# Performance work log

Hardware: AMD Instinct MI355X
Metric: run time of the kernel (lower is better)

The kernel has to match this reference:

```python
import jax, jax.numpy as jnp
import numpy as np
import math

B, T, C = 2, 2048, 1024
H = 16
D = C // H

def setup_inputs() -> dict:
    key = jax.random.key(0)
    k1, k2, k3, k4, k5 = jax.random.split(key, 5)
    scale = 0.02
    return {
        "x": jax.random.normal(k1, (B, T, C), dtype=jnp.float32),
        "w_attn": jax.random.normal(k2, (3 * C, C), dtype=jnp.float32) * scale,
        "b_attn": jax.random.normal(k3, (3 * C,), dtype=jnp.float32) * scale,
        "w_proj": jax.random.normal(k4, (C, C), dtype=jnp.float32) * scale,
        "b_proj": jax.random.normal(k5, (C,), dtype=jnp.float32) * scale,
    }

def reference(x, w_attn, b_attn, w_proj, b_proj):
    b, t, c = x.shape
    # c_attn: torch Linear -> x @ W.T + b, output [b, t, 3c]
    qkv = jnp.einsum('btc,fc->btf', x, w_attn) + b_attn
    # einops 'b t (a h d) -> a b h t d' with a=3, h=H
    qkv = qkv.reshape(b, t, 3, H, D).transpose(2, 0, 3, 1, 4)
    q, k, v = qkv[0], qkv[1], qkv[2]  # each [b, h, t, d]
    att = jnp.einsum('bhtd,bhsd->bhts', q, k) * (1.0 / math.sqrt(D))
    # causal mask: positions s > t are masked
    mask = jnp.tril(jnp.ones((t, t), dtype=bool))
    att = jnp.where(mask[None, None, :, :], att, jnp.float32(-jnp.inf))
    att = jax.nn.softmax(att, axis=-1)
    y = jnp.einsum('bhts,bhsd->bhtd', att, v)  # [b, h, t, d]
    y = y.transpose(0, 2, 1, 3).reshape(b, t, c)
    return jnp.einsum('btc,fc->btf', y, w_proj) + b_proj
```

## Files before the change

### kernel.cpp

```cpp
#include <hip/hip_runtime.h>
#include <hip/hip_bf16.h>
#include <stdint.h>

typedef unsigned short u16;
typedef __attribute__((ext_vector_type(8))) __bf16 bvec8;
typedef __attribute__((ext_vector_type(4))) float f32x4;
typedef __attribute__((ext_vector_type(16))) float f32x16;

__device__ __forceinline__ u16 f32_to_bf16(float f) {
    uint32_t u = __float_as_uint(f);
    u += 0x7fffu + ((u >> 16) & 1u);
    return (u16)(u >> 16);
}
__device__ __forceinline__ uint32_t pack_bf16x2(float lo, float hi) {
    union { __hip_bfloat162 h; uint32_t u; } c;
    c.h = __float22bfloat162_rn(make_float2(lo, hi));
    return c.u;
}

__device__ __forceinline__ void gl2lds16(const u16* g, u16* l) {
    void* gnc = const_cast<void*>((const void*)g);
    __builtin_amdgcn_global_load_lds(
        (__attribute__((address_space(1))) uint32_t*)gnc,
        (__attribute__((address_space(3))) uint32_t*)((void*)l),
        16, 0, 0);
}

__global__ __launch_bounds__(256) void cvt3(
    const float* __restrict__ a, int na4, const float* __restrict__ b, int nb4,
    const float* __restrict__ c, int nc4,
    u16* __restrict__ oa, u16* __restrict__ ob, u16* __restrict__ oc)
{
    int i = blockIdx.x * 256 + threadIdx.x;
    const float* src; u16* dst; int off;
    if (i < na4)             { src = a; dst = oa; off = i; }
    else if (i < na4 + nb4)  { src = b; dst = ob; off = i - na4; }
    else if (i < na4 + nb4 + nc4) { src = c; dst = oc; off = i - na4 - nb4; }
    else return;
    float4 v = ((const float4*)src)[off];
    ushort4 o;
    o.x = f32_to_bf16(v.x); o.y = f32_to_bf16(v.y);
    o.z = f32_to_bf16(v.z); o.w = f32_to_bf16(v.w);
    ((ushort4*)dst)[off] = o;
}

template <int BNt, bool OUT_BF16>
__global__ __launch_bounds__(256) void gemm_bt_bias(
    const u16* __restrict__ A, const u16* __restrict__ B,
    const float* __restrict__ bias, void* __restrict__ Cv,
    int M, int N, int K)
{
    constexpr int NT = BNt / 32;
    __shared__ __attribute__((aligned(16))) u16 As[128 * 32];
    __shared__ __attribute__((aligned(16))) u16 Bs[BNt * 32];

    const int tid = threadIdx.x, wave = tid >> 6, lane = tid & 63;
    const int col = lane & 15, quad = lane >> 4;
    const int m0 = blockIdx.y * 128, n0 = blockIdx.x * BNt;
    const int wm = (wave >> 1) * 64, wn = (wave & 1) * (BNt / 2);
    const int srow = lane >> 2, schunk = lane & 3;
    const u16* Ag = A + (size_t)(m0 + wave * 32) * K;

    f32x4 acc[4][NT];
#pragma unroll
    for (int i = 0; i < 4; i++)
#pragma unroll
        for (int j = 0; j < NT; j++) acc[i][j] = f32x4{0.f, 0.f, 0.f, 0.f};

    for (int k0 = 0; k0 < K; k0 += 32) {
        __syncthreads();
        gl2lds16(Ag + (size_t)(srow)      * K + k0 + schunk * 8, &As[(wave * 2 + 0) * 512]);
        gl2lds16(Ag + (size_t)(16 + srow) * K + k0 + schunk * 8, &As[(wave * 2 + 1) * 512]);
        if constexpr (BNt == 128) {
            const u16* Bg = B + (size_t)(n0 + wave * 32) * K;
            gl2lds16(Bg + (size_t)(srow)      * K + k0 + schunk * 8, &Bs[(wave * 2 + 0) * 512]);
            gl2lds16(Bg + (size_t)(16 + srow) * K + k0 + schunk * 8, &Bs[(wave * 2 + 1) * 512]);
        } else {
            const u16* Bg = B + (size_t)(n0 + wave * 16) * K;
            gl2lds16(Bg + (size_t)(srow)      * K + k0 + schunk * 8, &Bs[wave * 512]);
        }
        __syncthreads();

        bvec8 af[4], bfv[NT];
#pragma unroll
        for (int mt = 0; mt < 4; mt++)  af[mt]  = *(const bvec8*)&As[(wm + mt * 16 + col) * 32 + quad * 8];
#pragma unroll
        for (int nt = 0; nt < NT; nt++) bfv[nt] = *(const bvec8*)&Bs[(wn + nt * 16 + col) * 32 + quad * 8];
#pragma unroll
        for (int mt = 0; mt < 4; mt++)
#pragma unroll
            for (int nt = 0; nt < NT; nt++)
                acc[mt][nt] = __builtin_amdgcn_mfma_f32_16x16x32_bf16(af[mt], bfv[nt], acc[mt][nt], 0, 0, 0);
    }

#pragma unroll
    for (int mt = 0; mt < 4; mt++) {
#pragma unroll
        for (int r = 0; r < 4; r++) {
            const int m = m0 + wm + mt * 16 + quad * 4 + r;
#pragma unroll
            for (int nt = 0; nt < NT; nt++) {
                const int n = n0 + wn + nt * 16 + col;
                float v = acc[mt][nt][r] + bias[n];
                if (OUT_BF16) ((u16*)Cv)[(size_t)m * N + n] = f32_to_bf16(v);
                else          ((float*)Cv)[(size_t)m * N + n] = v;
            }
        }
    }
}

__global__ __launch_bounds__(256) void transpose_v(const u16* __restrict__ qkv,
                                                   u16* __restrict__ vT)
{
    __shared__ u16 Ts[64 * 74];
    const int tid = threadIdx.x;
    const int t0 = blockIdx.x * 64, h = blockIdx.y, b = blockIdx.z;
    const u16* src = qkv + (size_t)b * 2048 * 3072 + 2048 + h * 64;
#pragma unroll
    for (int k2 = 0; k2 < 2; k2++) {
        int c = k2 * 256 + tid, tl = c >> 3, ch = c & 7;
        *(uint4*)&Ts[tl * 74 + ch * 8] = *(const uint4*)(src + (size_t)(t0 + tl) * 3072 + ch * 8);
    }
    __syncthreads();
    u16* dst = vT + (size_t)((b * 16 + h) * 64) * 2048;
#pragma unroll
    for (int k2 = 0; k2 < 2; k2++) {
        int c = k2 * 256 + tid, d = c >> 3, tch = c & 7;
        u16 tmp[8];
#pragma unroll
        for (int j2 = 0; j2 < 8; j2++) {
            int p  = tch * 8 + j2;
            int sl = (p & 32) | ((p & 1) << 4) | ((p >> 1) & 15);
            tmp[j2] = Ts[sl * 74 + d];
        }
        *(uint4*)&dst[(size_t)d * 2048 + t0 + tch * 8] = *(const uint4*)tmp;
    }
}

__global__ __launch_bounds__(256) void attn_kernel(const u16* __restrict__ qkv,
                                                   const u16* __restrict__ vT,
                                                   u16* __restrict__ Y)
{
    __shared__ __attribute__((aligned(16))) u16 Qs[64 * 64];
    __shared__ __attribute__((aligned(16))) u16 Ks[2][64 * 64];
    __shared__ __attribute__((aligned(16))) u16 Vs[2][64 * 64];
    __shared__ __attribute__((aligned(16))) float Obuf[2][64][36];
    __shared__ __attribute__((aligned(16))) float Lbuf[2][2][32];

    const int tid = threadIdx.x, wave = tid >> 6, lane = tid & 63;
    const int l31 = lane & 31, hi = lane >> 5;
    const int wq = wave >> 1, ws = wave & 1;

    const int g = blockIdx.x;
    const int b = g >> 4, h = g & 15;
    const int s_idx = blockIdx.y;

    const u16* qb = qkv + (size_t)b * 2048 * 3072;
    const u16* vb = vT + (size_t)g * 64 * 2048;

    const int c0 = wave * 64 + lane, c1 = 256 + c0;
    const int r0 = c0 >> 3, p0c = c0 & 7, r1 = c1 >> 3, p1c = c1 & 7;
    const int sw0 = (p0c ^ (r0 & 7)) * 8, sw1 = (p1c ^ (r1 & 7)) * 8;

    const int q_lane = wq * 32 + l31;
    const int s_lane = ws * 32 + l31;

#pragma unroll
    for (int phase = 0; phase < 2; ++phase) {
        const int qt = phase ? (31 - s_idx) : s_idx;
        const int q0 = qt * 64;

        __syncthreads();
        gl2lds16(qb + (size_t)(q0 + r0) * 3072 + h * 64 + sw0, &Qs[wave * 512]);
        gl2lds16(qb + (size_t)(q0 + r1) * 3072 + h * 64 + sw1, &Qs[2048 + wave * 512]);
        gl2lds16(qb + (size_t)(r0) * 3072 + 1024 + h * 64 + sw0, &Ks[0][wave * 512]);
        gl2lds16(qb + (size_t)(r1) * 3072 + 1024 + h * 64 + sw1, &Ks[0][2048 + wave * 512]);
        gl2lds16(vb + (size_t)r0 * 2048 + sw0, &Vs[0][wave * 512]);
        gl2lds16(vb + (size_t)r1 * 2048 + sw1, &Vs[0][2048 + wave * 512]);
        asm volatile("s_waitcnt vmcnt(4)" ::: "memory");
        asm volatile("s_barrier" ::: "memory");

        bvec8 qf[4];
#pragma unroll
        for (int c = 0; c < 4; c++)
            qf[c] = *(const bvec8*)&Qs[q_lane * 64 + (((c * 2 + hi) ^ (q_lane & 7)) * 8)];

        float l_acc = 0.f;
        f32x16 o0, o1;
#pragma unroll
        for (int i = 0; i < 16; i++) { o0[i] = 0.f; o1[i] = 0.f; }

        for (int kt = 0; kt <= qt; ++kt) {
            const int cur = kt & 1;
            if (kt < qt) {
                const int s0n = (kt + 1) * 64, nb2 = cur ^ 1;
                gl2lds16(qb + (size_t)(s0n + r0) * 3072 + 1024 + h * 64 + sw0, &Ks[nb2][wave * 512]);
                gl2lds16(qb + (size_t)(s0n + r1) * 3072 + 1024 + h * 64 + sw1, &Ks[nb2][2048 + wave * 512]);
                gl2lds16(vb + (size_t)r0 * 2048 + s0n + sw0, &Vs[nb2][wave * 512]);
                gl2lds16(vb + (size_t)r1 * 2048 + s0n + sw1, &Vs[nb2][2048 + wave * 512]);
                asm volatile("s_waitcnt vmcnt(4)" ::: "memory");
            } else {
                asm volatile("s_waitcnt vmcnt(0)" ::: "memory");
            }
            asm volatile("s_barrier" ::: "memory");

            const bool diag = (kt == qt);
            if (!(diag && wq == 0 && ws == 1)) {
                f32x16 sv;
#pragma unroll
                for (int i = 0; i < 16; i++) sv[i] = 0.f;
#pragma unroll
                for (int c = 0; c < 4; c++) {
                    bvec8 kf = *(const bvec8*)&Ks[cur][s_lane * 64 + (((c * 2 + hi) ^ (s_lane & 7)) * 8)];
                    sv = __builtin_amdgcn_mfma_f32_32x32x16_bf16(kf, qf[c], sv, 0, 0, 0);
                }

                float pv[16];
                if (diag) {
                    const int s_base = kt * 64 + ws * 32 + 4 * hi;
                    const int q_act  = q0 + wq * 32 + l31;
#pragma unroll
                    for (int i = 0; i < 16; i++) {
                        float p = exp2f(sv[i] * 0.1803368801f);
                        int s_act = s_base + (i & 3) + 8 * (i >> 2);
                        if (s_act > q_act) p = 0.f;
                        pv[i] = p;
                    }
                } else {
#pragma unroll
                    for (int i = 0; i < 16; i++)
                        pv[i] = exp2f(sv[i] * 0.1803368801f);
                }
                {
                    float t0a = (pv[0] + pv[1]) + (pv[2] + pv[3]);
                    float t1a = (pv[4] + pv[5]) + (pv[6] + pv[7]);
                    float t2a = (pv[8] + pv[9]) + (pv[10] + pv[11]);
                    float t3a = (pv[12] + pv[13]) + (pv[14] + pv[15]);
                    l_acc += (t0a + t1a) + (t2a + t3a);
                }

                uint32_t w[8];
#pragma unroll
                for (int i = 0; i < 8; i++) w[i] = pack_bf16x2(pv[i], pv[i + 8]);
                union { uint32_t u[4]; bvec8 v; } pf0, pf1;
                pf0.u[0] = w[0]; pf0.u[1] = w[1]; pf0.u[2] = w[2]; pf0.u[3] = w[3];
                pf1.u[0] = w[4]; pf1.u[1] = w[5]; pf1.u[2] = w[6]; pf1.u[3] = w[7];

#pragma unroll
                for (int ch = 0; ch < 2; ch++) {
                    bvec8 pf = ch ? pf1.v : pf0.v;
                    const int lc = ws * 4 + ch * 2 + hi;
                    const int d0r = l31;
                    bvec8 vf0 = *(const bvec8*)&Vs[cur][d0r * 64 + ((lc ^ (d0r & 7)) * 8)];
                    o0 = __builtin_amdgcn_mfma_f32_32x32x16_bf16(pf, vf0, o0, 0, 0, 0);
                    const int d1r = 32 + l31;
                    bvec8 vf1 = *(const bvec8*)&Vs[cur][d1r * 64 + ((lc ^ (d1r & 7)) * 8)];
                    o1 = __builtin_amdgcn_mfma_f32_32x32x16_bf16(pf, vf1, o1, 0, 0, 0);
                }
            }
            asm volatile("s_barrier" ::: "memory");
        }

        l_acc += __shfl_xor(l_acc, 32);
        __syncthreads();
        if (lane < 32) Lbuf[ws][wq][lane] = l_acc;
        if (ws == 0) {
#pragma unroll
            for (int nt = 0; nt < 2; nt++) {
                const int d = nt * 32 + l31;
#pragma unroll
                for (int g4 = 0; g4 < 4; g4++) {
                    f32x4 v;
#pragma unroll
                    for (int j = 0; j < 4; j++) v[j] = nt ? o1[g4 * 4 + j] : o0[g4 * 4 + j];
                    *(f32x4*)&Obuf[wq][d][8 * g4 + 4 * hi] = v;
                }
            }
        }
        __syncthreads();
        if (ws == 1) {
            float inv[16];
#pragma unroll
            for (int g4 = 0; g4 < 4; g4++) {
                f32x4 la = *(const f32x4*)&Lbuf[0][wq][8 * g4 + 4 * hi];
                f32x4 lb = *(const f32x4*)&Lbuf[1][wq][8 * g4 + 4 * hi];
#pragma unroll
                for (int j = 0; j < 4; j++) inv[g4 * 4 + j] = 1.0f / (la[j] + lb[j]);
            }
#pragma unroll
            for (int nt = 0; nt < 2; nt++) {
                const int d = nt * 32 + l31;
#pragma unroll
                for (int g4 = 0; g4 < 4; g4++) {
                    f32x4 po = *(const f32x4*)&Obuf[wq][d][8 * g4 + 4 * hi];
#pragma unroll
                    for (int j = 0; j < 4; j++) {
                        const int i = g4 * 4 + j;
                        float val = ((nt ? o1[i] : o0[i]) + po[j]) * inv[i];
                        const int t = q0 + wq * 32 + 8 * g4 + 4 * hi + j;
                        Y[(size_t)(b * 2048 + t) * 1024 + h * 64 + d] = f32_to_bf16(val);
                    }
                }
            }
        }
    }
}

extern "C" void kernel_launch(void* const* d_in, const int* in_sizes, int n_in,
                              void* d_out, int out_size, void* d_ws, size_t ws_size,
                              hipStream_t stream) {
    const float* x      = (const float*)d_in[0];
    const float* w_attn = (const float*)d_in[1];
    const float* b_attn = (const float*)d_in[2];
    const float* w_proj = (const float*)d_in[3];
    const float* b_proj = (const float*)d_in[4];
    float* out = (float*)d_out;

    u16* xb  = (u16*)d_ws;
    u16* wab = xb  + (size_t)4096 * 1024;
    u16* wpb = wab + (size_t)3072 * 1024;
    u16* qkv = wpb + (size_t)1024 * 1024;
    u16* y   = qkv + (size_t)4096 * 3072;
    u16* vT  = xb;

    const int na4 = 4096 * 1024 / 4, nb4 = 3072 * 1024 / 4, nc4 = 1024 * 1024 / 4;
    cvt3<<<(na4 + nb4 + nc4 + 255) / 256, 256, 0, stream>>>(
        x, na4, w_attn, nb4, w_proj, nc4, xb, wab, wpb);

    dim3 g1(3072 / 128, 4096 / 128);
    gemm_bt_bias<128, true><<<g1, 256, 0, stream>>>(xb, wab, b_attn, qkv, 4096, 3072, 1024);

    dim3 gt(32, 16, 2);
    transpose_v<<<gt, 256, 0, stream>>>(qkv, vT);

    dim3 g2(32, 16, 1);
    attn_kernel<<<g2, 256, 0, stream>>>(qkv, vT, y);

    dim3 g3(1024 / 64, 4096 / 128);
    gemm_bt_bias<64, false><<<g3, 256, 0, stream>>>(y, wpb, b_proj, out, 4096, 1024, 1024);
}
```

Measured before the change: 194.3 us.

## Use 128-row query tiles with one wave per 32 queries in attention

The attention kernel now gives each block a 128-query tile, with each of the four waves owning 32 query rows across the full 64-key tile. This replaces the old 64-query tiles, where two waves split the keys and merged partial outputs through shared memory. Load balancing now pairs tile j with tile 23-j. Each K/V tile loaded into shared memory is reused by twice as many queries, and the cross-wave Obuf/Lbuf reduction and its syncthreads are gone. In exchange there are fewer blocks (a grid y of 16 is implied), which may lower occupancy, and each wave holds more registers.

Result: slower. 210.1 us (+8.2%).

```diff
diff --git a/kernel.cpp b/kernel.cpp
--- a/kernel.cpp
+++ b/kernel.cpp
@@ -141,167 +141,143 @@
                                                    const u16* __restrict__ vT,
                                                    u16* __restrict__ Y)
 {
-    __shared__ __attribute__((aligned(16))) u16 Qs[64 * 64];
+    __shared__ __attribute__((aligned(16))) u16 Qs[128 * 64];
     __shared__ __attribute__((aligned(16))) u16 Ks[2][64 * 64];
     __shared__ __attribute__((aligned(16))) u16 Vs[2][64 * 64];
-    __shared__ __attribute__((aligned(16))) float Obuf[2][64][36];
-    __shared__ __attribute__((aligned(16))) float Lbuf[2][2][32];
+    __shared__ __attribute__((aligned(16))) float Lbuf[4][32];
 
     const int tid = threadIdx.x, wave = tid >> 6, lane = tid & 63;
     const int l31 = lane & 31, hi = lane >> 5;
-    const int wq = wave >> 1, ws = wave & 1;
 
     const int g = blockIdx.x;
     const int b = g >> 4, h = g & 15;
-    const int s_idx = blockIdx.y;
+    const int j = blockIdx.y;
+    const int qt = (j < 8) ? j : (23 - j);
+    const int q0 = qt * 128;
+    const int nkt = 2 * qt + 2;
 
     const u16* qb = qkv + (size_t)b * 2048 * 3072;
     const u16* vb = vT + (size_t)g * 64 * 2048;
 
+#pragma unroll
+    for (int g4 = 0; g4 < 4; g4++) {
+        int c = g4 * 256 + wave * 64 + lane;
+        int r = c >> 3, ch = c & 7;
+        gl2lds16(qb + (size_t)(q0 + r) * 3072 + h * 64 + ((ch ^ (r & 7)) * 8),
+                 &Qs[g4 * 2048 + wave * 512]);
+    }
     const int c0 = wave * 64 + lane, c1 = 256 + c0;
-    const int r0 = c0 >> 3, p0c = c0 & 7, r1 = c1 >> 3, p1c = c1 & 7;
-    const int sw0 = (p0c ^ (r0 & 7)) * 8, sw1 = (p1c ^ (r1 & 7)) * 8;
-
-    const int q_lane = wq * 32 + l31;
-    const int s_lane = ws * 32 + l31;
-
-#pragma unroll
-    for (int phase = 0; phase < 2; ++phase) {
-        const int qt = phase ? (31 - s_idx) : s_idx;
-        const int q0 = qt * 64;
-
-        __syncthreads();
-        gl2lds16(qb + (size_t)(q0 + r0) * 3072 + h * 64 + sw0, &Qs[wave * 512]);
-        gl2lds16(qb + (size_t)(q0 + r1) * 3072 + h * 64 + sw1, &Qs[2048 + wave * 512]);
-        gl2lds16(qb + (size_t)(r0) * 3072 + 1024 + h * 64 + sw0, &Ks[0][wave * 512]);
-        gl2lds16(qb + (size_t)(r1) * 3072 + 1024 + h * 64 + sw1, &Ks[0][2048 + wave * 512]);
-        gl2lds16(vb + (size_t)r0 * 2048 + sw0, &Vs[0][wave * 512]);
-        gl2lds16(vb + (size_t)r1 * 2048 + sw1, &Vs[0][2048 + wave * 512]);
-        asm volatile("s_waitcnt vmcnt(4)" ::: "memory");
+    const int r0 = c0 >> 3, r1 = c1 >> 3;
+    const int sw0 = ((c0 & 7) ^ (r0 & 7)) * 8, sw1 = ((c1 & 7) ^ (r1 & 7)) * 8;
+
+    gl2lds16(qb + (size_t)(r0) * 3072 + 1024 + h * 64 + sw0, &Ks[0][wave * 512]);
+    gl2lds16(qb + (size_t)(r1) * 3072 + 1024 + h * 64 + sw1, &Ks[0][2048 + wave * 512]);
+    gl2lds16(vb + (size_t)r0 * 2048 + sw0, &Vs[0][wave * 512]);
+    gl2lds16(vb + (size_t)r1 * 2048 + sw1, &Vs[0][2048 + wave * 512]);
+    asm volatile("s_waitcnt vmcnt(4)" ::: "memory");
+    asm volatile("s_barrier" ::: "memory");
+
+    const int q_lane = wave * 32 + l31;
+    bvec8 qf[4];
+#pragma unroll
+    for (int c = 0; c < 4; c++)
+        qf[c] = *(const bvec8*)&Qs[q_lane * 64 + (((c * 2 + hi) ^ (q_lane & 7)) * 8)];
+
+    const int qmin  = q0 + wave * 32;
+    const int qmax  = qmin + 31;
+    const int q_act = qmin + l31;
+
+    float l_acc = 0.f;
+    f32x16 o0, o1;
+#pragma unroll
+    for (int i = 0; i < 16; i++) { o0[i] = 0.f; o1[i] = 0.f; }
+
+    for (int kt = 0; kt < nkt; ++kt) {
+        const int cur = kt & 1;
+        if (kt + 1 < nkt) {
+            const int s0n = (kt + 1) * 64, nb2 = cur ^ 1;
+            gl2lds16(qb + (size_t)(s0n + r0) * 3072 + 1024 + h * 64 + sw0, &Ks[nb2][wave * 512]);
+            gl2lds16(qb + (size_t)(s0n + r1) * 3072 + 1024 + h * 64 + sw1, &Ks[nb2][2048 + wave * 512]);
+            gl2lds16(vb + (size_t)r0 * 2048 + s0n + sw0, &Vs[nb2][wave * 512]);
+            gl2lds16(vb + (size_t)r1 * 2048 + s0n + sw1, &Vs[nb2][2048 + wave * 512]);
+            asm volatile("s_waitcnt vmcnt(4)" ::: "memory");
+        } else {
+            asm volatile("s_waitcnt vmcnt(0)" ::: "memory");
+        }
         asm volatile("s_barrier" ::: "memory");
 
-        bvec8 qf[4];
-#pragma unroll
-        for (int c = 0; c < 4; c++)
-            qf[c] = *(const bvec8*)&Qs[q_lane * 64 + (((c * 2 + hi) ^ (q_lane & 7)) * 8)];
-
-        float l_acc = 0.f;
-        f32x16 o0, o1;
-#pragma unroll
-        for (int i = 0; i < 16; i++) { o0[i] = 0.f; o1[i] = 0.f; }
-
-        for (int kt = 0; kt <= qt; ++kt) {
-            const int cur = kt & 1;
-            if (kt < qt) {
-                const int s0n = (kt + 1) * 64, nb2 = cur ^ 1;
-                gl2lds16(qb + (size_t)(s0n + r0) * 3072 + 1024 + h * 64 + sw0, &Ks[nb2][wave * 512]);
-                gl2lds16(qb + (size_t)(s0n + r1) * 3072 + 1024 + h * 64 + sw1, &Ks[nb2][2048 + wave * 512]);
-                gl2lds16(vb + (size_t)r0 * 2048 + s0n + sw0, &Vs[nb2][wave * 512]);
-                gl2lds16(vb + (size_t)r1 * 2048 + s0n + sw1, &Vs[nb2][2048 + wave * 512]);
-                asm volatile("s_waitcnt vmcnt(4)" ::: "memory");
-            } else {
-                asm volatile("s_waitcnt vmcnt(0)" ::: "memory");
-            }
-            asm volatile("s_barrier" ::: "memory");
-
-            const bool diag = (kt == qt);
-            if (!(diag && wq == 0 && ws == 1)) {
-                f32x16 sv;
-#pragma unroll
-                for (int i = 0; i < 16; i++) sv[i] = 0.f;
-#pragma unroll
-                for (int c = 0; c < 4; c++) {
-                    bvec8 kf = *(const bvec8*)&Ks[cur][s_lane * 64 + (((c * 2 + hi) ^ (s_lane & 7)) * 8)];
-                    sv = __builtin_amdgcn_mfma_f32_32x32x16_bf16(kf, qf[c], sv, 0, 0, 0);
+        const int s_t0 = kt * 64;
+        if (s_t0 <= qmax) {
+            f32x16 sv0, sv1;
+#pragma unroll
+            for (int i = 0; i < 16; i++) { sv0[i] = 0.f; sv1[i] = 0.f; }
+#pragma unroll
+            for (int c = 0; c < 4; c++) {
+                bvec8 kf = *(const bvec8*)&Ks[cur][l31 * 64 + (((c * 2 + hi) ^ (l31 & 7)) * 8)];
+                sv0 = __builtin_amdgcn_mfma_f32_32x32x16_bf16(kf, qf[c], sv0, 0, 0, 0);
+            }
+#pragma unroll
+            for (int c = 0; c < 4; c++) {
+                const int rr = 32 + l31;
+                bvec8 kf = *(const bvec8*)&Ks[cur][rr * 64 + (((c * 2 + hi) ^ (rr & 7)) * 8)];
+                sv1 = __builtin_amdgcn_mfma_f32_32x32x16_bf16(kf, qf[c], sv1, 0, 0, 0);
+            }
+
+            const bool msk = (s_t0 + 63 > qmin);
+            float pv0[16], pv1[16];
+#pragma unroll
+            for (int i = 0; i < 16; i++) {
+                float p0 = __expf(sv0[i] * 0.125f);
+                float p1 = __expf(sv1[i] * 0.125f);
+                if (msk) {
+                    const int srow = s_t0 + (i & 3) + 8 * (i >> 2) + 4 * hi;
+                    if (srow > q_act)      p0 = 0.f;
+                    if (srow + 32 > q_act) p1 = 0.f;
                 }
-
-                float pv[16];
-                if (diag) {
-                    const int s_base = kt * 64 + ws * 32 + 4 * hi;
-                    const int q_act  = q0 + wq * 32 + l31;
-#pragma unroll
-                    for (int i = 0; i < 16; i++) {
-                        float p = exp2f(sv[i] * 0.1803368801f);
-                        int s_act = s_base + (i & 3) + 8 * (i >> 2);
-                        if (s_act > q_act) p = 0.f;
-                        pv[i] = p;
-                    }
-                } else {
-#pragma unroll
-                    for (int i = 0; i < 16; i++)
-                        pv[i] = exp2f(sv[i] * 0.1803368801f);
-                }
-                {
-                    float t0a = (pv[0] + pv[1]) + (pv[2] + pv[3]);
-                    float t1a = (pv[4] + pv[5]) + (pv[6] + pv[7]);
-                    float t2a = (pv[8] + pv[9]) + (pv[10] + pv[11]);
-                    float t3a = (pv[12] + pv[13]) + (pv[14] + pv[15]);
-                    l_acc += (t0a + t1a) + (t2a + t3a);
-                }
-
-                uint32_t w[8];
-#pragma unroll
-                for (int i = 0; i < 8; i++) w[i] = pack_bf16x2(pv[i], pv[i + 8]);
-                union { uint32_t u[4]; bvec8 v; } pf0, pf1;
-                pf0.u[0] = w[0]; pf0.u[1] = w[1]; pf0.u[2] = w[2]; pf0.u[3] = w[3];
-                pf1.u[0] = w[4]; pf1.u[1] = w[5]; pf1.u[2] = w[6]; pf1.u[3] = w[7];
-
-#pragma unroll
-                for (int ch = 0; ch < 2; ch++) {
-                    bvec8 pf = ch ? pf1.v : pf0.v;
-                    const int lc = ws * 4 + ch * 2 + hi;
-                    const int d0r = l31;
-                    bvec8 vf0 = *(const bvec8*)&Vs[cur][d0r * 64 + ((lc ^ (d0r & 7)) * 8)];
-                    o0 = __builtin_amdgcn_mfma_f32_32x32x16_bf16(pf, vf0, o0, 0, 0, 0);
-                    const int d1r = 32 + l31;
-                    bvec8 vf1 = *(const bvec8*)&Vs[cur][d1r * 64 + ((lc ^ (d1r & 7)) * 8)];
-                    o1 = __builtin_amdgcn_mfma_f32_32x32x16_bf16(pf, vf1, o1, 0, 0, 0);
-                }
-            }
-            asm volatile("s_barrier" ::: "memory");
-        }
-
-        l_acc += __shfl_xor(l_acc, 32);
-        __syncthreads();
-        if (lane < 32) Lbuf[ws][wq][lane] = l_acc;
-        if (ws == 0) {
-#pragma unroll
-            for (int nt = 0; nt < 2; nt++) {
-                const int d = nt * 32 + l31;
-#pragma unroll
-                for (int g4 = 0; g4 < 4; g4++) {
-                    f32x4 v;
-#pragma unroll
-                    for (int j = 0; j < 4; j++) v[j] = nt ? o1[g4 * 4 + j] : o0[g4 * 4 + j];
-                    *(f32x4*)&Obuf[wq][d][8 * g4 + 4 * hi] = v;
-                }
-            }
-        }
-        __syncthreads();
-        if (ws == 1) {
-            float inv[16];
-#pragma unroll
-            for (int g4 = 0; g4 < 4; g4++) {
-                f32x4 la = *(const f32x4*)&Lbuf[0][wq][8 * g4 + 4 * hi];
-                f32x4 lb = *(const f32x4*)&Lbuf[1][wq][8 * g4 + 4 * hi];
-#pragma unroll
-                for (int j = 0; j < 4; j++) inv[g4 * 4 + j] = 1.0f / (la[j] + lb[j]);
-            }
-#pragma unroll
-            for (int nt = 0; nt < 2; nt++) {
-                const int d = nt * 32 + l31;
-#pragma unroll
-                for (int g4 = 0; g4 < 4; g4++) {
-                    f32x4 po = *(const f32x4*)&Obuf[wq][d][8 * g4 + 4 * hi];
-#pragma unroll
-                    for (int j = 0; j < 4; j++) {
-                        const int i = g4 * 4 + j;
-                        float val = ((nt ? o1[i] : o0[i]) + po[j]) * inv[i];
-                        const int t = q0 + wq * 32 + 8 * g4 + 4 * hi + j;
-                        Y[(size_t)(b * 2048 + t) * 1024 + h * 64 + d] = f32_to_bf16(val);
-                    }
-                }
-            }
+                pv0[i] = p0; pv1[i] = p1;
+                l_acc += p0 + p1;
+            }
+
+            union { uint32_t u[4]; bvec8 v; } pf[4];
+#pragma unroll
+            for (int i2 = 0; i2 < 4; i2++) {
+                pf[0].u[i2] = pack_bf16x2(pv0[i2],     pv0[i2 + 8]);
+                pf[1].u[i2] = pack_bf16x2(pv0[i2 + 4], pv0[i2 + 12]);
+                pf[2].u[i2] = pack_bf16x2(pv1[i2],     pv1[i2 + 8]);
+                pf[3].u[i2] = pack_bf16x2(pv1[i2 + 4], pv1[i2 + 12]);
+            }
+
+#pragma unroll
+            for (int jc = 0; jc < 4; jc++) {
+                const int lc = jc * 2 + hi;
+                bvec8 vf0 = *(const bvec8*)&Vs[cur][l31 * 64 + ((lc ^ (l31 & 7)) * 8)];
+                o0 = __builtin_amdgcn_mfma_f32_32x32x16_bf16(pf[jc].v, vf0, o0, 0, 0, 0);
+                const int rr = 32 + l31;
+                bvec8 vf1 = *(const bvec8*)&Vs[cur][rr * 64 + ((lc ^ (rr & 7)) * 8)];
+                o1 = __builtin_amdgcn_mfma_f32_32x32x16_bf16(pf[jc].v, vf1, o1, 0, 0, 0);
+            }
+        }
+        asm volatile("s_barrier" ::: "memory");
+    }
+
+    l_acc += __shfl_xor(l_acc, 32);
+    if (hi == 0) Lbuf[wave][l31] = l_acc;
+    float inv[16];
+#pragma unroll
+    for (int g4 = 0; g4 < 4; g4++) {
+        f32x4 lv = *(const f32x4*)&Lbuf[wave][g4 * 8 + 4 * hi];
+#pragma unroll
+        for (int jj = 0; jj < 4; jj++) inv[g4 * 4 + jj] = 1.0f / lv[jj];
+    }
+#pragma unroll
+    for (int g4 = 0; g4 < 4; g4++) {
+#pragma unroll
+        for (int jj = 0; jj < 4; jj++) {
+            const int i = g4 * 4 + jj;
+            const int t = q0 + wave * 32 + g4 * 8 + 4 * hi + jj;
+            u16* yrow = Y + (size_t)(b * 2048 + t) * 1024 + h * 64;
+            yrow[l31]      = f32_to_bf16(o0[i] * inv[i]);
+            yrow[32 + l31] = f32_to_bf16(o1[i] * inv[i]);
         }
     }
 }
```
